# Kernel optimization log

Hardware: AMD Instinct MI355X
Metric: run time of the kernel (lower is better)

## Reference

```python
import jax, jax.numpy as jnp
import numpy as np

TOPK = 13
ALPHA = 1.0
BETA = 6.0
NUM_CLASSES = 80
EPS = 1e-9


def _make_boxes(key, shape, max_half):
    # shape = (..., 4): build valid x1y1x2y2 boxes inside a 640x640 image
    kc, ks = jax.random.split(key)
    centers = jax.random.uniform(kc, shape[:-1] + (2,), minval=30.0, maxval=610.0)
    halves = jax.random.uniform(ks, shape[:-1] + (2,), minval=2.0, maxval=max_half)
    return jnp.concatenate([centers - halves, centers + halves], axis=-1)


def setup_inputs() -> dict:
    key = jax.random.key(0)
    k1, k2, k3, k4, k5 = jax.random.split(key, 5)
    B, L, C, n = 16, 8400, NUM_CLASSES, 128
    pred_scores = jax.random.uniform(k1, (B, L, C), dtype=jnp.float32)
    pred_bboxes = _make_boxes(k2, (B, L, 4), 60.0)
    anchor_points = jax.random.uniform(k3, (L, 2), minval=0.0, maxval=640.0)
    gt_labels = jax.random.randint(k4, (B, n), 0, C, dtype=jnp.int32)
    gt_bboxes = _make_boxes(k5, (B, n, 4), 120.0)
    pad_gt_mask = jnp.ones((B, n, 1), dtype=jnp.float32)
    return {"pred_scores": pred_scores, "pred_bboxes": pred_bboxes,
            "anchor_points": anchor_points, "gt_labels": gt_labels,
            "gt_bboxes": gt_bboxes, "pad_gt_mask": pad_gt_mask}


def _batch_iou(box1, box2, eps=1e-9):
    # box1: [B, n, 4], box2: [B, L, 4] -> iou [B, n, L]
    b1 = box1[:, :, None]  # [B,n,1,4]
    b2 = box2[:, None]     # [B,1,L,4]
    x1y1 = jnp.maximum(b1[..., 0:2], b2[..., 0:2])
    x2y2 = jnp.minimum(b1[..., 2:4], b2[..., 2:4])
    overlap = jnp.prod(jnp.clip(x2y2 - x1y1, 0.0), axis=-1)
    area1 = jnp.prod(jnp.clip(b1[..., 2:4] - b1[..., 0:2], 0.0), axis=-1)
    area2 = jnp.prod(jnp.clip(b2[..., 2:4] - b2[..., 0:2], 0.0), axis=-1)
    return overlap / (area1 + area2 - overlap + eps)


def _points_in_bboxes(points, bboxes, eps=EPS):
    # points: [L,2], bboxes: [B,n,4] -> [B,n,L] float
    x = points[None, None, :, 0]
    y = points[None, None, :, 1]
    xmin = bboxes[..., 0:1]; ymin = bboxes[..., 1:2]
    xmax = bboxes[..., 2:3]; ymax = bboxes[..., 3:4]
    l = x - xmin; t = y - ymin; r = xmax - x; b = ymax - y
    d = jnp.minimum(jnp.minimum(l, t), jnp.minimum(r, b))
    return (d > eps).astype(bboxes.dtype)


def _gather_topk(metrics, topk, topk_mask):
    # metrics: [B,n,L] -> one-hot membership of per-gt topk anchors [B,n,L]
    L = metrics.shape[-1]
    _, topk_idxs = jax.lax.top_k(metrics, topk)          # [B,n,topk]
    is_in_topk = jax.nn.one_hot(topk_idxs, L, dtype=metrics.dtype).sum(-2)
    return is_in_topk * topk_mask


def reference(pred_scores, pred_bboxes, anchor_points, gt_labels, gt_bboxes, pad_gt_mask):
    B, n, _ = gt_bboxes.shape
    L = pred_bboxes.shape[1]
    # pairwise IoU between gts and predicted boxes: [B,n,L]
    ious = _batch_iou(gt_bboxes, pred_bboxes)
    # per-gt class scores gathered from pred_scores: [B,n,L]
    scores_cl = jnp.transpose(pred_scores, (0, 2, 1))                 # [B,C,L]
    bbox_cls_scores = jnp.take_along_axis(scores_cl, gt_labels[:, :, None].astype(jnp.int32), axis=1)
    # task-aligned metric
    alignment = (bbox_cls_scores ** ALPHA) * (ious ** BETA)
    is_in_gts = _points_in_bboxes(anchor_points, gt_bboxes)           # [B,n,L]
    is_in_topk = _gather_topk(alignment * is_in_gts, TOPK, pad_gt_mask)
    mask_positive = is_in_topk * is_in_gts * pad_gt_mask              # [B,n,L]
    # resolve anchors assigned to multiple gts: keep max-IoU gt
    mask_pos_sum = mask_positive.sum(-2)                              # [B,L]
    is_max_iou = jnp.transpose(jax.nn.one_hot(jnp.argmax(ious, axis=-2), n, dtype=ious.dtype), (0, 2, 1))
    mask_positive = jnp.where((mask_pos_sum[:, None, :] > 1), is_max_iou, mask_positive)
    mask_pos_sum = mask_positive.sum(-2)
    # assignment
    assigned_gt_index = jnp.argmax(mask_positive, axis=-2)            # [B,L]
    flat_idx = assigned_gt_index + jnp.arange(B, dtype=assigned_gt_index.dtype)[:, None] * n
    assigned_labels = jnp.reshape(gt_labels, (-1,))[flat_idx]
    assigned_labels = jnp.where(mask_pos_sum > 0, assigned_labels, NUM_CLASSES)
    assigned_bboxes = jnp.reshape(gt_bboxes, (-1, 4))[flat_idx]       # [B,L,4]
    assigned_scores = jax.nn.one_hot(assigned_labels, NUM_CLASSES + 1, dtype=pred_scores.dtype)[..., :NUM_CLASSES]
    # rescale scores by normalized alignment metric
    align_m = alignment * mask_positive
    max_metric = align_m.max(-1, keepdims=True)                       # [B,n,1]
    max_iou = (ious * mask_positive).max(-1, keepdims=True)           # [B,n,1]
    align_m = (align_m / (max_metric + EPS)) * max_iou
    assigned_scores = assigned_scores * align_m.max(-2)[..., None]    # [B,L,C]
    return assigned_labels, assigned_bboxes, assigned_scores
```

## Files before the change

kernel.cpp:

```cpp
#include <hip/hip_runtime.h>
#include <stdint.h>

#define BB   16
#define NGT  128
#define LL   8400
#define CC   80
#define KTOP 13
#define CAP  2048
#define FEPS 1e-9f

typedef float vfloat4 __attribute__((ext_vector_type(4)));

__device__ __forceinline__ float iou_f(float4 g, float4 p) {
    float ix0 = fmaxf(g.x, p.x);
    float iy0 = fmaxf(g.y, p.y);
    float ix1 = fminf(g.z, p.z);
    float iy1 = fminf(g.w, p.w);
    float ow = fmaxf(ix1 - ix0, 0.0f);
    float oh = fmaxf(iy1 - iy0, 0.0f);
    float ov = ow * oh;
    float a1 = fmaxf(g.z - g.x, 0.0f) * fmaxf(g.w - g.y, 0.0f);
    float a2 = fmaxf(p.z - p.x, 0.0f) * fmaxf(p.w - p.y, 0.0f);
    return ov / (a1 + a2 - ov + FEPS);
}

__global__ __launch_bounds__(256) void topk_kernel(
    const float*  __restrict__ pred_scores,
    const float4* __restrict__ pred_bboxes,
    const float2* __restrict__ anchors,
    const int*    __restrict__ gt_labels,
    const float4* __restrict__ gt_bboxes,
    int* __restrict__ claim_count,
    int* __restrict__ claimant)
{
    int row  = blockIdx.x;
    int b    = row >> 7;
    int tid  = threadIdx.x;
    int wave = tid >> 6;
    int lane = tid & 63;

    float4 g   = gt_bboxes[row];
    int label  = gt_labels[row];
    const float*  sc = pred_scores + (size_t)b * LL * CC + label;
    const float4* pb = pred_bboxes + (size_t)b * LL;

    __shared__ int s_cnt;
    __shared__ int s_list[CAP];
    __shared__ unsigned long long wkeys[4 * KTOP];
    __shared__ int s_pick[KTOP];
    if (tid == 0) s_cnt = 0;
    __syncthreads();

    for (int j = tid; j < LL; j += 256) {
        float2 ap = anchors[j];
        float d = fminf(fminf(ap.x - g.x, ap.y - g.y),
                        fminf(g.z - ap.x, g.w - ap.y));
        bool inside = d > FEPS;
        unsigned long long mask = __ballot(inside);
        if (mask) {
            int leader = __ffsll((unsigned long long)mask) - 1;
            int base = 0;
            if (lane == leader) base = atomicAdd(&s_cnt, __popcll(mask));
            base = __shfl(base, leader, 64);
            if (inside) {
                int slot = base + __popcll(mask & ((1ull << lane) - 1ull));
                if (slot < CAP) s_list[slot] = j;
            }
        }
    }
    __syncthreads();
    int c = s_cnt; if (c > CAP) c = CAP;

    unsigned long long keys[KTOP];
#pragma unroll
    for (int k = 0; k < KTOP; ++k) keys[k] = 0ull;

    if (tid < 64) {
        float2 ap = anchors[tid];
        float d = fminf(fminf(ap.x - g.x, ap.y - g.y),
                        fminf(g.z - ap.x, g.w - ap.y));
        if (!(d > FEPS)) keys[0] = (unsigned)(~(unsigned)tid);
    }

    for (int t = tid; t < c; t += 256) {
        int j = s_list[t];
        float4 p  = pb[j];
        float iou = iou_f(g, p);
        unsigned long long key = (unsigned)(~(unsigned)j);
        if (iou > 0.0f) {
            float s   = sc[(size_t)j * CC];
            float i2  = iou * iou;
            float metric = s * (i2 * i2 * i2);
            key |= ((unsigned long long)__float_as_uint(metric) << 32);
        }
        if (key > keys[KTOP - 1]) {
            keys[KTOP - 1] = key;
#pragma unroll
            for (int k = KTOP - 1; k > 0; --k) {
                unsigned long long a = keys[k - 1], cc2 = keys[k];
                keys[k - 1] = (cc2 > a) ? cc2 : a;
                keys[k]     = (cc2 > a) ? a : cc2;
            }
        }
    }

    for (int r = 0; r < KTOP; ++r) {
        unsigned long long head = keys[0];
        unsigned long long m = head;
#pragma unroll
        for (int off = 1; off < 64; off <<= 1) {
            unsigned long long o = __shfl_xor(m, off, 64);
            if (o > m) m = o;
        }
        if (head == m && m != 0ull) {
#pragma unroll
            for (int k = 0; k < KTOP - 1; ++k) keys[k] = keys[k + 1];
            keys[KTOP - 1] = 0ull;
        }
        if (lane == 0) wkeys[wave * KTOP + r] = m;
    }
    __syncthreads();

    if (wave == 0) {
        unsigned long long k1 = (lane < 4 * KTOP) ? wkeys[lane] : 0ull;
        for (int r = 0; r < KTOP; ++r) {
            unsigned long long m = k1;
#pragma unroll
            for (int off = 1; off < 64; off <<= 1) {
                unsigned long long o = __shfl_xor(m, off, 64);
                if (o > m) m = o;
            }
            if (k1 == m && m != 0ull) k1 = 0ull;
            if (lane == 0) s_pick[r] = (int)(~(unsigned)(m & 0xFFFFFFFFull));
        }
    }
    __syncthreads();

    if (tid < KTOP) {
        int j = s_pick[tid];
        float2 ap = anchors[j];
        float d = fminf(fminf(ap.x - g.x, ap.y - g.y),
                        fminf(g.z - ap.x, g.w - ap.y));
        if (d > FEPS) {
            atomicAdd(claim_count + b * LL + j, 1);
            atomicMax(claimant + b * LL + j, row & (NGT - 1));
        }
    }
}

__global__ __launch_bounds__(256) void resolve_kernel(
    const float*  __restrict__ pred_scores,
    const float4* __restrict__ pred_bboxes,
    const int*    __restrict__ gt_labels,
    const float4* __restrict__ gt_bboxes,
    const int*    __restrict__ claim_count,
    const int*    __restrict__ claimant,
    int*      __restrict__ assigned_gt,
    float*    __restrict__ align_anchor,
    unsigned* __restrict__ max_metric,
    unsigned* __restrict__ max_iou,
    float*    __restrict__ out_labels,
    float4*   __restrict__ out_bboxes)
{
    int b = blockIdx.y;
    int j = blockIdx.x * 256 + threadIdx.x;

    __shared__ float4 gbox[NGT];
    __shared__ int    glab[NGT];
    if (threadIdx.x < NGT) {
        gbox[threadIdx.x] = gt_bboxes[b * NGT + threadIdx.x];
        glab[threadIdx.x] = gt_labels[b * NGT + threadIdx.x];
    }
    __syncthreads();
    if (j >= LL) return;

    int idx = b * LL + j;
    int cnt = claim_count[idx];
    int g = -1;
    float4 p = pred_bboxes[(size_t)b * LL + j];

    if (cnt == 1) {
        g = claimant[idx];
    } else if (cnt > 1) {
        float best = -1.0f;
        int   bi   = 0;
        for (int i = 0; i < NGT; ++i) {
            float iou = iou_f(gbox[i], p);
            if (iou > best) { best = iou; bi = i; }
        }
        g = bi;
    }
    assigned_gt[idx] = g;

    int label; float4 bb;
    if (g >= 0) {
        float iou = iou_f(gbox[g], p);
        float s   = pred_scores[((size_t)b * LL + j) * CC + glab[g]];
        float i2  = iou * iou;
        float al  = s * (i2 * i2 * i2);
        align_anchor[idx] = al;
        atomicMax(max_metric + b * NGT + g, __float_as_uint(al));
        atomicMax(max_iou    + b * NGT + g, __float_as_uint(iou));
        label = glab[g];
        bb    = gbox[g];
    } else {
        label = CC;
        bb    = gbox[0];
    }
    out_labels[idx] = (float)label;
    out_bboxes[idx] = bb;
}

__global__ __launch_bounds__(256) void score_kernel(
    const int*    __restrict__ gt_labels,
    const int*    __restrict__ assigned_gt,
    const float*  __restrict__ align_anchor,
    const unsigned* __restrict__ max_metric,
    const unsigned* __restrict__ max_iou,
    float*  __restrict__ out_scores)
{
    int t = blockIdx.x * 256 + threadIdx.x;
    __shared__ int   s_lab[256];
    __shared__ float s_f[256];

    int b = t / LL;
    int g = assigned_gt[t];
    int label = CC;
    float f = 0.0f;
    if (g >= 0) {
        label = gt_labels[b * NGT + g];
        float mm = __uint_as_float(max_metric[b * NGT + g]);
        float mi = __uint_as_float(max_iou[b * NGT + g]);
        f = align_anchor[t] / (mm + FEPS) * mi;
    }
    s_lab[threadIdx.x] = label;
    s_f[threadIdx.x]   = f;
    __syncthreads();

    vfloat4* outs = (vfloat4*)(out_scores + (size_t)blockIdx.x * 256 * CC);
    for (int i = threadIdx.x; i < 256 * CC / 4; i += 256) {
        int anchor = i / (CC / 4);
        int c4     = i % (CC / 4);
        int lab    = s_lab[anchor];
        vfloat4 v = {0.f, 0.f, 0.f, 0.f};
        int rel = lab - c4 * 4;
        if (rel >= 0 && rel < 4) v[rel] = s_f[anchor];
        __builtin_nontemporal_store(v, outs + i);
    }
}

extern "C" void kernel_launch(void* const* d_in, const int* in_sizes, int n_in,
                              void* d_out, int out_size, void* d_ws, size_t ws_size,
                              hipStream_t stream)
{
    const float*  pred_scores = (const float*)d_in[0];
    const float4* pred_bboxes = (const float4*)d_in[1];
    const float2* anchors     = (const float2*)d_in[2];
    const int*    gt_labels   = (const int*)d_in[3];
    const float4* gt_bboxes   = (const float4*)d_in[4];

    char* w = (char*)d_ws;
    int*      claim_count  = (int*)(w);
    int*      claimant     = (int*)(w + 537600);
    unsigned* max_metric   = (unsigned*)(w + 1075200);
    unsigned* max_iou      = (unsigned*)(w + 1083392);
    int*      assigned_gt  = (int*)(w + 1091584);
    float*    align_anchor = (float*)(w + 1629184);

    float*  out        = (float*)d_out;
    float*  out_labels = out;
    float4* out_bboxes = (float4*)(out + (size_t)BB * LL);
    float*  out_scores = out + (size_t)BB * LL * 5;

    (void)hipMemsetAsync(w, 0, 1091584, stream);

    topk_kernel<<<BB * NGT, 256, 0, stream>>>(
        pred_scores, pred_bboxes, anchors, gt_labels, gt_bboxes,
        claim_count, claimant);

    dim3 gridC((LL + 255) / 256, BB);
    resolve_kernel<<<gridC, 256, 0, stream>>>(
        pred_scores, pred_bboxes, gt_labels, gt_bboxes,
        claim_count, claimant, assigned_gt, align_anchor, max_metric, max_iou,
        out_labels, out_bboxes);

    score_kernel<<<(BB * LL) / 256, 256, 0, stream>>>(
        gt_labels, assigned_gt, align_anchor, max_metric, max_iou, out_scores);
}
```

Baseline: 100.7 us.

## Map one ground-truth box per wave and keep inside-masks in registers

The top-k kernel now assigns one GT row per wavefront instead of one per 256-thread block. Anchor-inside tests are packed into per-lane 64-bit bitmasks held in registers rather than compacted into a shared-memory list. The cross-wave merge through shared memory and the block barriers go away, and lane 0 issues the claim atomics directly. In exchange each wave scans all anchors alone with uneven per-lane work, and the old CAP limit on candidates is removed.

```diff
diff --git a/kernel.cpp b/kernel.cpp
--- a/kernel.cpp
+++ b/kernel.cpp
@@ -6,7 +6,6 @@
 #define LL   8400
 #define CC   80
 #define KTOP 13
-#define CAP  2048
 #define FEPS 1e-9f
 
 typedef float vfloat4 __attribute__((ext_vector_type(4)));
@@ -33,77 +32,80 @@
     int* __restrict__ claim_count,
     int* __restrict__ claimant)
 {
-    int row  = blockIdx.x;
+    int wave = threadIdx.x >> 6;
+    int lane = threadIdx.x & 63;
+    int row  = blockIdx.x * 4 + wave;
     int b    = row >> 7;
-    int tid  = threadIdx.x;
-    int wave = tid >> 6;
-    int lane = tid & 63;
-
-    float4 g   = gt_bboxes[row];
-    int label  = gt_labels[row];
+    int i_gt = row & (NGT - 1);
+
+    float4 g  = gt_bboxes[row];
+    int label = gt_labels[row];
     const float*  sc = pred_scores + (size_t)b * LL * CC + label;
     const float4* pb = pred_bboxes + (size_t)b * LL;
 
-    __shared__ int s_cnt;
-    __shared__ int s_list[CAP];
-    __shared__ unsigned long long wkeys[4 * KTOP];
-    __shared__ int s_pick[KTOP];
-    if (tid == 0) s_cnt = 0;
-    __syncthreads();
-
-    for (int j = tid; j < LL; j += 256) {
+    unsigned long long m0 = 0ull, m1 = 0ull, m2 = 0ull;
+#pragma unroll 8
+    for (int it = 0; it < 64; ++it) {
+        int j = lane + (it << 6);
         float2 ap = anchors[j];
         float d = fminf(fminf(ap.x - g.x, ap.y - g.y),
                         fminf(g.z - ap.x, g.w - ap.y));
-        bool inside = d > FEPS;
-        unsigned long long mask = __ballot(inside);
-        if (mask) {
-            int leader = __ffsll((unsigned long long)mask) - 1;
-            int base = 0;
-            if (lane == leader) base = atomicAdd(&s_cnt, __popcll(mask));
-            base = __shfl(base, leader, 64);
-            if (inside) {
-                int slot = base + __popcll(mask & ((1ull << lane) - 1ull));
-                if (slot < CAP) s_list[slot] = j;
-            }
-        }
-    }
-    __syncthreads();
-    int c = s_cnt; if (c > CAP) c = CAP;
-
-    unsigned long long keys[KTOP];
-#pragma unroll
-    for (int k = 0; k < KTOP; ++k) keys[k] = 0ull;
-
-    if (tid < 64) {
-        float2 ap = anchors[tid];
+        m0 |= ((unsigned long long)(d > FEPS)) << it;
+    }
+#pragma unroll 8
+    for (int it = 0; it < 64; ++it) {
+        int j = lane + ((it + 64) << 6);
+        float2 ap = anchors[j];
         float d = fminf(fminf(ap.x - g.x, ap.y - g.y),
                         fminf(g.z - ap.x, g.w - ap.y));
-        if (!(d > FEPS)) keys[0] = (unsigned)(~(unsigned)tid);
-    }
-
-    for (int t = tid; t < c; t += 256) {
-        int j = s_list[t];
-        float4 p  = pb[j];
-        float iou = iou_f(g, p);
-        unsigned long long key = (unsigned)(~(unsigned)j);
-        if (iou > 0.0f) {
-            float s   = sc[(size_t)j * CC];
-            float i2  = iou * iou;
-            float metric = s * (i2 * i2 * i2);
-            key |= ((unsigned long long)__float_as_uint(metric) << 32);
-        }
-        if (key > keys[KTOP - 1]) {
-            keys[KTOP - 1] = key;
-#pragma unroll
-            for (int k = KTOP - 1; k > 0; --k) {
-                unsigned long long a = keys[k - 1], cc2 = keys[k];
-                keys[k - 1] = (cc2 > a) ? cc2 : a;
-                keys[k]     = (cc2 > a) ? a : cc2;
+        m1 |= ((unsigned long long)(d > FEPS)) << it;
+    }
+#pragma unroll
+    for (int it = 0; it < 4; ++it) {
+        int j = lane + ((it + 128) << 6);
+        if (j < LL) {
+            float2 ap = anchors[j];
+            float d = fminf(fminf(ap.x - g.x, ap.y - g.y),
+                            fminf(g.z - ap.x, g.w - ap.y));
+            m2 |= ((unsigned long long)(d > FEPS)) << it;
+        }
+    }
+
+    unsigned long long keys[KTOP];
+#pragma unroll
+    for (int k = 0; k < KTOP; ++k) keys[k] = 0ull;
+
+    if (!(m0 & 1ull)) keys[0] = (unsigned)(~(unsigned)lane);
+
+#pragma unroll
+    for (int w = 0; w < 3; ++w) {
+        unsigned long long mask = (w == 0) ? m0 : (w == 1) ? m1 : m2;
+        int itbase = w << 6;
+        while (mask) {
+            int p = __ffsll(mask) - 1;
+            mask &= mask - 1ull;
+            int j = lane + ((itbase + p) << 6);
+            float4 pbx = pb[j];
+            float iou = iou_f(g, pbx);
+            unsigned long long key = (unsigned)(~(unsigned)j);
+            if (iou > 0.0f) {
+                float s  = sc[(size_t)j * CC];
+                float i2 = iou * iou;
+                key |= ((unsigned long long)__float_as_uint(s * (i2 * i2 * i2)) << 32);
             }
-        }
-    }
-
+            if (key > keys[KTOP - 1]) {
+                keys[KTOP - 1] = key;
+#pragma unroll
+                for (int k = KTOP - 1; k > 0; --k) {
+                    unsigned long long a = keys[k - 1], c2 = keys[k];
+                    keys[k - 1] = (c2 > a) ? c2 : a;
+                    keys[k]     = (c2 > a) ? a : c2;
+                }
+            }
+        }
+    }
+
+    int base = b * LL;
     for (int r = 0; r < KTOP; ++r) {
         unsigned long long head = keys[0];
         unsigned long long m = head;
@@ -117,33 +119,15 @@
             for (int k = 0; k < KTOP - 1; ++k) keys[k] = keys[k + 1];
             keys[KTOP - 1] = 0ull;
         }
-        if (lane == 0) wkeys[wave * KTOP + r] = m;
-    }
-    __syncthreads();
-
-    if (wave == 0) {
-        unsigned long long k1 = (lane < 4 * KTOP) ? wkeys[lane] : 0ull;
-        for (int r = 0; r < KTOP; ++r) {
-            unsigned long long m = k1;
-#pragma unroll
-            for (int off = 1; off < 64; off <<= 1) {
-                unsigned long long o = __shfl_xor(m, off, 64);
-                if (o > m) m = o;
+        if (lane == 0 && m != 0ull) {
+            int j = (int)(~(unsigned)(m & 0xFFFFFFFFull));
+            float2 ap = anchors[j];
+            float d = fminf(fminf(ap.x - g.x, ap.y - g.y),
+                            fminf(g.z - ap.x, g.w - ap.y));
+            if (d > FEPS) {
+                atomicAdd(claim_count + base + j, 1);
+                atomicMax(claimant + base + j, i_gt);
             }
-            if (k1 == m && m != 0ull) k1 = 0ull;
-            if (lane == 0) s_pick[r] = (int)(~(unsigned)(m & 0xFFFFFFFFull));
-        }
-    }
-    __syncthreads();
-
-    if (tid < KTOP) {
-        int j = s_pick[tid];
-        float2 ap = anchors[j];
-        float d = fminf(fminf(ap.x - g.x, ap.y - g.y),
-                        fminf(g.z - ap.x, g.w - ap.y));
-        if (d > FEPS) {
-            atomicAdd(claim_count + b * LL + j, 1);
-            atomicMax(claimant + b * LL + j, row & (NGT - 1));
         }
     }
 }
@@ -274,7 +258,7 @@
 
     (void)hipMemsetAsync(w, 0, 1091584, stream);
 
-    topk_kernel<<<BB * NGT, 256, 0, stream>>>(
+    topk_kernel<<<BB * NGT / 4, 256, 0, stream>>>(
         pred_scores, pred_bboxes, anchors, gt_labels, gt_bboxes,
         claim_count, claimant);
 
```

Result: faster. 96.90 us (-3.8%).
